# Kernel optimization log

Hardware: AMD Instinct MI355X
Metric: run time of the kernel (lower is better)

Reference implementation:

```python
import jax, jax.numpy as jnp
import numpy as np

N = 100_000      # nodes
E = 1_600_000    # edges
D = 128          # in_dim == hidden_dim
H = 4            # heads
HD = D // H      # per-head dim = 32
B = 8            # graphs in batch
TD = 128         # time_dim
NEG_SLOPE = 0.2
EPS = 1e-5


def _gelu(v):
    return jax.nn.gelu(v, approximate=False)  # torch default erf-GELU


def _layernorm(v, g, b):
    mu = jnp.mean(v, axis=-1, keepdims=True)
    var = jnp.var(v, axis=-1, keepdims=True)
    return (v - mu) * jax.lax.rsqrt(var + EPS) * g + b


def setup_inputs() -> dict:
    key = jax.random.key(0)
    ks = jax.random.split(key, 24)
    s = 1.0 / np.sqrt(D)
    inp = {
        "x": jax.random.normal(ks[0], (N, D), jnp.float32),
        "src": jax.random.randint(ks[1], (E,), 0, N),
        "dst": jax.random.randint(ks[2], (E,), 0, N),
        "graph_ids": jnp.sort(jax.random.randint(ks[3], (N,), 0, B)),
        "time_emb": jax.random.normal(ks[4], (B, TD), jnp.float32),
        # GATv2 params
        "Wsrc": jax.random.normal(ks[5], (D, D), jnp.float32) * s,
        "bsrc": jnp.zeros((D,), jnp.float32),
        "Wdst": jax.random.normal(ks[6], (D, D), jnp.float32) * s,
        "bdst": jnp.zeros((D,), jnp.float32),
        "attn": jax.random.normal(ks[7], (H, HD), jnp.float32) * (1.0 / np.sqrt(HD)),
        "gat_bias": jnp.zeros((D,), jnp.float32),
        # LayerNorms
        "ln1_g": jnp.ones((D,), jnp.float32), "ln1_b": jnp.zeros((D,), jnp.float32),
        "ln2_g": jnp.ones((D,), jnp.float32), "ln2_b": jnp.zeros((D,), jnp.float32),
        # time MLP
        "tW": jax.random.normal(ks[8], (TD, D), jnp.float32) * (1.0 / np.sqrt(TD)),
        "tb": jnp.zeros((D,), jnp.float32),
        # FFN
        "W1": jax.random.normal(ks[9], (D, 2 * D), jnp.float32) * s,
        "b1": jnp.zeros((2 * D,), jnp.float32),
        "W2": jax.random.normal(ks[10], (2 * D, D), jnp.float32) * (1.0 / np.sqrt(2 * D)),
        "b2": jnp.zeros((D,), jnp.float32),
    }
    return inp


def reference(x, src, dst, graph_ids, time_emb, Wsrc, bsrc, Wdst, bdst, attn,
              gat_bias, ln1_g, ln1_b, ln2_g, ln2_b, tW, tb, W1, b1, W2, b2):
    h = _layernorm(x, ln1_g, ln1_b)                       # [N, D]
    # GATv2Conv (share_weights=False, residual=False, activation=gelu)
    feat_src = (h @ Wsrc + bsrc).reshape(N, H, HD)        # [N, H, HD]
    feat_dst = (h @ Wdst + bdst).reshape(N, H, HD)
    e = feat_src[src] + feat_dst[dst]                     # [E, H, HD]
    e = jnp.where(e > 0, e, NEG_SLOPE * e)                # leaky_relu
    scores = jnp.einsum("ehd,hd->eh", e, attn)            # [E, H]
    # segment softmax over incoming edges of each dst node
    m = jax.ops.segment_max(scores, dst, num_segments=N)  # [N, H]
    ex = jnp.exp(scores - m[dst])
    denom = jax.ops.segment_sum(ex, dst, num_segments=N)  # [N, H]
    alpha = ex / denom[dst]                               # [E, H]
    msg = feat_src[src] * alpha[:, :, None]               # [E, H, HD]
    rst = jax.ops.segment_sum(msg, dst, num_segments=N)   # [N, H, HD]
    rst = _gelu(rst + gat_bias.reshape(H, HD))
    h = rst.reshape(N, D)                                 # flatten(1)
    # ragged time-embedding expand: time_condition[graph_of(node)]
    time_cond = _gelu(time_emb @ tW + tb)                 # [B, D]
    h = h + time_cond[graph_ids]
    h = h + x                                             # proj = Identity (in_dim == hidden_dim)
    h2 = _layernorm(h, ln2_g, ln2_b)
    h2 = _gelu(h2 @ W1 + b1) @ W2 + b2                    # FFN
    return h + h2
```

## Files before the change

### kernel.cpp

```cpp
#include <hip/hip_runtime.h>
#include <hip/hip_bf16.h>


#define RB 16
#define NEG_SLOPE 0.2f
#define LN_EPS 1e-5f

typedef __attribute__((ext_vector_type(8))) short short8v;
typedef __attribute__((ext_vector_type(4))) float floatx4;

__device__ __forceinline__ float gelu_erf(float v) {
    return 0.5f * v * (1.0f + erff(v * 0.70710678118654752f));
}
__device__ __forceinline__ unsigned short f2bf(float f) {
    unsigned int u = __float_as_uint(f);
    u += 0x7fffu + ((u >> 16) & 1u);
    return (unsigned short)(u >> 16);
}
__device__ __forceinline__ float bf2f(unsigned short u) {
    return __uint_as_float(((unsigned int)u) << 16);
}

__global__ __launch_bounds__(256) void pack_w(
    const float* __restrict__ W, unsigned short* __restrict__ P, int K, int C)
{
    int tid = blockIdx.x * 256 + threadIdx.x;
    int total = (K >> 5) * (C >> 4) * 64;
    if (tid >= total) return;
    int lane = tid & 63;
    int f = tid >> 6;
    int nkt = K >> 5;
    int nt = f / nkt, kt = f - nt * nkt;
    int col = nt * 16 + (lane & 15);
    int k0 = kt * 32 + 8 * (lane >> 4);
    short8v v;
    #pragma unroll
    for (int i = 0; i < 8; ++i)
        v[i] = (short)f2bf(W[(size_t)(k0 + i) * C + col]);
    *(short8v*)(P + (size_t)tid * 8) = v;
}

__global__ __launch_bounds__(256) void ln1_dual_gemm(
    const float* __restrict__ x,
    const float* __restrict__ ln_g, const float* __restrict__ ln_b,
    const unsigned short* __restrict__ pWs, const float* __restrict__ bsrc,
    const unsigned short* __restrict__ pWd, const float* __restrict__ bdst,
    unsigned short* __restrict__ fs, float* __restrict__ fd, int nrows)
{
    __shared__ __align__(16) float hs[RB][132];
    __shared__ __align__(16) unsigned short pa[4 * 64 * 8];
    __shared__ float s_mu[RB], s_rs[RB];

    const int tid  = threadIdx.x;
    const int row0 = blockIdx.x * RB;
    const int lane = tid & 63;
    const int w    = tid >> 6;

    #pragma unroll
    for (int i = 0; i < 2; ++i) {
        int f   = tid + i * 256;
        int row = f >> 5;
        int c0  = (f & 31) * 4;
        float4 v = make_float4(0.f, 0.f, 0.f, 0.f);
        if (row0 + row < nrows) v = *(const float4*)(x + (size_t)(row0 + row) * 128 + c0);
        *(float4*)&hs[row][c0] = v;
    }
    __syncthreads();

    {
        const int ln = lane;
        #pragma unroll
        for (int rr = 0; rr < 4; ++rr) {
            int row = w * 4 + rr;
            float v0 = hs[row][ln * 2], v1 = hs[row][ln * 2 + 1];
            float s = v0 + v1, sq = v0 * v0 + v1 * v1;
            #pragma unroll
            for (int m = 32; m; m >>= 1) { s += __shfl_xor(s, m); sq += __shfl_xor(sq, m); }
            if (ln == 0) {
                float mu  = s * (1.0f / 128.0f);
                float var = sq * (1.0f / 128.0f) - mu * mu;
                s_mu[row] = mu;
                s_rs[row] = rsqrtf(var + LN_EPS);
            }
        }
    }
    __syncthreads();

    {
        const int kt  = w;
        const int row = lane & 15;
        const int k0  = kt * 32 + 8 * (lane >> 4);
        float mu = s_mu[row], rs = s_rs[row];
        float4 u  = *(float4*)&hs[row][k0];
        float4 v  = *(float4*)&hs[row][k0 + 4];
        float4 g0 = *(const float4*)&ln_g[k0];
        float4 g1 = *(const float4*)&ln_g[k0 + 4];
        float4 c0 = *(const float4*)&ln_b[k0];
        float4 c1 = *(const float4*)&ln_b[k0 + 4];
        short8v pv;
        pv[0] = (short)f2bf((u.x - mu) * rs * g0.x + c0.x);
        pv[1] = (short)f2bf((u.y - mu) * rs * g0.y + c0.y);
        pv[2] = (short)f2bf((u.z - mu) * rs * g0.z + c0.z);
        pv[3] = (short)f2bf((u.w - mu) * rs * g0.w + c0.w);
        pv[4] = (short)f2bf((v.x - mu) * rs * g1.x + c1.x);
        pv[5] = (short)f2bf((v.y - mu) * rs * g1.y + c1.y);
        pv[6] = (short)f2bf((v.z - mu) * rs * g1.z + c1.z);
        pv[7] = (short)f2bf((v.w - mu) * rs * g1.w + c1.w);
        *(short8v*)&pa[(kt * 64 + lane) * 8] = pv;
    }
    __syncthreads();

    short8v a[4];
    #pragma unroll
    for (int kt = 0; kt < 4; ++kt)
        a[kt] = *(const short8v*)&pa[(kt * 64 + lane) * 8];

    #pragma unroll
    for (int j = 0; j < 2; ++j) {
        const int nt = 2 * w + j;
        floatx4 aS = {0.f, 0.f, 0.f, 0.f};
        floatx4 aD = {0.f, 0.f, 0.f, 0.f};
        #pragma unroll
        for (int kt = 0; kt < 4; ++kt) {
            short8v bS = *(const short8v*)(pWs + (size_t)((nt * 4 + kt) * 64 + lane) * 8);
            aS = __builtin_amdgcn_mfma_f32_16x16x32_bf16(a[kt], bS, aS, 0, 0, 0);
            short8v bD = *(const short8v*)(pWd + (size_t)((nt * 4 + kt) * 64 + lane) * 8);
            aD = __builtin_amdgcn_mfma_f32_16x16x32_bf16(a[kt], bD, aD, 0, 0, 0);
        }
        const int col = nt * 16 + (lane & 15);
        const float bS0 = bsrc[col], bD0 = bdst[col];
        #pragma unroll
        for (int r = 0; r < 4; ++r) {
            int grow = row0 + 4 * (lane >> 4) + r;
            if (grow < nrows) {
                fs[(size_t)grow * 128 + col] = f2bf(aS[r] + bS0);
                fd[(size_t)grow * 128 + col] = aD[r] + bD0;
            }
        }
    }
}

__global__ __launch_bounds__(256) void time_mlp(
    const float* __restrict__ temb, const float* __restrict__ tW,
    const float* __restrict__ tb, float* __restrict__ tc, int B)
{
    __shared__ float te[8 * 128];
    int tid = threadIdx.x;
    for (int i = tid; i < B * 128; i += 256) te[i] = temb[i];
    __syncthreads();
    int c = tid & 127, half = tid >> 7;
    for (int b = half * 4; b < half * 4 + 4; ++b) {
        if (b >= B) break;
        float acc = 0.f;
        for (int k = 0; k < 128; ++k) acc = fmaf(te[b * 128 + k], tW[k * 128 + c], acc);
        tc[b * 128 + c] = gelu_erf(acc + tb[c]);
    }
}

__global__ __launch_bounds__(256) void csr_rank(
    const int* __restrict__ dst, int* __restrict__ deg, int* __restrict__ rank, int E)
{
    int e = blockIdx.x * 256 + threadIdx.x;
    if (e < E) rank[e] = atomicAdd(&deg[dst[e]], 1);
}

__global__ __launch_bounds__(256) void scan_blocks(
    const int* __restrict__ deg, int* __restrict__ rs, int* __restrict__ btot, int N)
{
    __shared__ int wtot[4];
    const int t    = threadIdx.x;
    const int idx  = blockIdx.x * 1024 + t * 4;
    int d0 = 0, d1 = 0, d2 = 0, d3 = 0;
    if (idx + 3 < N) {
        int4 v = *(const int4*)(deg + idx);
        d0 = v.x; d1 = v.y; d2 = v.z; d3 = v.w;
    } else {
        if (idx     < N) d0 = deg[idx];
        if (idx + 1 < N) d1 = deg[idx + 1];
        if (idx + 2 < N) d2 = deg[idx + 2];
        if (idx + 3 < N) d3 = deg[idx + 3];
    }
    const int ts = d0 + d1 + d2 + d3;
    const int lane = t & 63, w = t >> 6;
    int incl = ts;
    #pragma unroll
    for (int m = 1; m < 64; m <<= 1) { int u = __shfl_up(incl, m); if (lane >= m) incl += u; }
    if (lane == 63) wtot[w] = incl;
    __syncthreads();
    int woff = 0;
    #pragma unroll
    for (int i = 0; i < 4; ++i) woff += (i < w) ? wtot[i] : 0;
    const int p = woff + incl - ts;
    if (idx + 3 < N) {
        int4 o;
        o.x = p; o.y = p + d0; o.z = p + d0 + d1; o.w = p + d0 + d1 + d2;
        *(int4*)(rs + idx) = o;
    } else {
        if (idx     < N) rs[idx]     = p;
        if (idx + 1 < N) rs[idx + 1] = p + d0;
        if (idx + 2 < N) rs[idx + 2] = p + d0 + d1;
        if (idx + 3 < N) rs[idx + 3] = p + d0 + d1 + d2;
    }
    if (t == 255) btot[blockIdx.x] = woff + incl;
}

__global__ __launch_bounds__(64) void scan_tops(
    int* __restrict__ btot, int nb, int* __restrict__ rs, int N, int E)
{
    const int lane = threadIdx.x;
    int a0 = (2 * lane     < nb) ? btot[2 * lane]     : 0;
    int a1 = (2 * lane + 1 < nb) ? btot[2 * lane + 1] : 0;
    const int ts = a0 + a1;
    int incl = ts;
    #pragma unroll
    for (int m = 1; m < 64; m <<= 1) { int u = __shfl_up(incl, m); if (lane >= m) incl += u; }
    const int ex = incl - ts;
    if (2 * lane     < nb) btot[2 * lane]     = ex;
    if (2 * lane + 1 < nb) btot[2 * lane + 1] = ex + a0;
    if (lane == 0) rs[N] = E;
}

__global__ __launch_bounds__(256) void scan_add(
    int* __restrict__ rs, const int* __restrict__ btot, int N)
{
    int i = blockIdx.x * 256 + threadIdx.x;
    if (i < N) rs[i] += btot[i >> 10];
}

__global__ __launch_bounds__(256) void csr_fill(
    const int* __restrict__ dst, const int* __restrict__ src,
    const int* __restrict__ rs, const int* __restrict__ rank,
    int* __restrict__ srcSorted, int E)
{
    int e = blockIdx.x * 256 + threadIdx.x;
    if (e < E) srcSorted[rs[dst[e]] + rank[e]] = src[e];
}

__global__ __launch_bounds__(256) void gat_gather(
    const unsigned short* __restrict__ fs, float* __restrict__ fd,
    const float* __restrict__ x,
    const int* __restrict__ srcSorted, const int* __restrict__ rs,
    const float* __restrict__ attn, const float* __restrict__ gat_bias,
    const int* __restrict__ gid, const float* __restrict__ tc, int N)
{
    const int lane = threadIdx.x & 63;
    const int wib  = threadIdx.x >> 6;
    const int n    = blockIdx.x * 4 + wib;
    if (n >= N) return;

    const int g   = lane >> 4;
    const int l16 = lane & 15;
    const int d0  = l16 * 8;

    float c1[8], c2[8], vd[8];
    {
        float4 a0 = *(const float4*)(attn + d0);
        float4 a1 = *(const float4*)(attn + d0 + 4);
        c1[0] = 0.6f * a0.x; c2[0] = 0.4f * a0.x;
        c1[1] = 0.6f * a0.y; c2[1] = 0.4f * a0.y;
        c1[2] = 0.6f * a0.z; c2[2] = 0.4f * a0.z;
        c1[3] = 0.6f * a0.w; c2[3] = 0.4f * a0.w;
        c1[4] = 0.6f * a1.x; c2[4] = 0.4f * a1.x;
        c1[5] = 0.6f * a1.y; c2[5] = 0.4f * a1.y;
        c1[6] = 0.6f * a1.z; c2[6] = 0.4f * a1.z;
        c1[7] = 0.6f * a1.w; c2[7] = 0.4f * a1.w;
        float4 v0 = *(const float4*)(fd + (size_t)n * 128 + d0);
        float4 v1 = *(const float4*)(fd + (size_t)n * 128 + d0 + 4);
        vd[0] = v0.x; vd[1] = v0.y; vd[2] = v0.z; vd[3] = v0.w;
        vd[4] = v1.x; vd[5] = v1.y; vd[6] = v1.z; vd[7] = v1.w;
    }

    const int lo = rs[n], hi = rs[n + 1];
    const int T  = (hi - lo + 3) >> 2;

    float den = 0.f;
    float w[8];
    #pragma unroll
    for (int j = 0; j < 8; ++j) w[j] = 0.f;

    int i = lo + g;
    bool vA = (i < hi);
    int sA = vA ? srcSorted[i] : 0;
    uint4 rA = *(const uint4*)(fs + (size_t)sA * 128 + d0);

    for (int t = 0; t < T; ++t) {
        const int inx = i + 4;
        const bool vB = (inx < hi);
        const int sB = vB ? srcSorted[inx] : 0;
        uint4 rB = *(const uint4*)(fs + (size_t)sB * 128 + d0);

        float v[8];
        v[0] = __uint_as_float(rA.x << 16);
        v[1] = __uint_as_float(rA.x & 0xffff0000u);
        v[2] = __uint_as_float(rA.y << 16);
        v[3] = __uint_as_float(rA.y & 0xffff0000u);
        v[4] = __uint_as_float(rA.z << 16);
        v[5] = __uint_as_float(rA.z & 0xffff0000u);
        v[6] = __uint_as_float(rA.w << 16);
        v[7] = __uint_as_float(rA.w & 0xffff0000u);

        float p = 0.f;
        #pragma unroll
        for (int j = 0; j < 8; ++j) {
            float e = v[j] + vd[j];
            p = fmaf(c1[j], e, p);
            p = fmaf(c2[j], fabsf(e), p);
        }
        p += __shfl_xor(p, 1);
        p += __shfl_xor(p, 2);
        float exv = vA ? __expf(p) : 0.f;
        den += exv;
        #pragma unroll
        for (int j = 0; j < 8; ++j) w[j] = fmaf(exv, v[j], w[j]);

        vA = vB; rA = rB; i = inx;
    }

    den += __shfl_xor(den, 16);
    den += __shfl_xor(den, 32);
    #pragma unroll
    for (int j = 0; j < 8; ++j) {
        w[j] += __shfl_xor(w[j], 16);
        w[j] += __shfl_xor(w[j], 32);
    }

    if (g == 0) {
        const float inv = den > 0.f ? 1.0f / den : 0.f;
        const int gg = gid[n];
        float4 x0 = *(const float4*)(x  + (size_t)n * 128 + d0);
        float4 x1 = *(const float4*)(x  + (size_t)n * 128 + d0 + 4);
        float4 t0 = *(const float4*)(tc + (size_t)gg * 128 + d0);
        float4 t1 = *(const float4*)(tc + (size_t)gg * 128 + d0 + 4);
        float4 g0 = *(const float4*)(gat_bias + d0);
        float4 g1 = *(const float4*)(gat_bias + d0 + 4);
        float4 o0, o1;
        o0.x = gelu_erf(w[0] * inv + g0.x) + t0.x + x0.x;
        o0.y = gelu_erf(w[1] * inv + g0.y) + t0.y + x0.y;
        o0.z = gelu_erf(w[2] * inv + g0.z) + t0.z + x0.z;
        o0.w = gelu_erf(w[3] * inv + g0.w) + t0.w + x0.w;
        o1.x = gelu_erf(w[4] * inv + g1.x) + t1.x + x1.x;
        o1.y = gelu_erf(w[5] * inv + g1.y) + t1.y + x1.y;
        o1.z = gelu_erf(w[6] * inv + g1.z) + t1.z + x1.z;
        o1.w = gelu_erf(w[7] * inv + g1.w) + t1.w + x1.w;
        *(float4*)(fd + (size_t)n * 128 + d0)     = o0;
        *(float4*)(fd + (size_t)n * 128 + d0 + 4) = o1;
    }
}

__global__ __launch_bounds__(256) void combine_ffn(
    const float* __restrict__ hmg,
    const float* __restrict__ ln_g, const float* __restrict__ ln_b,
    const unsigned short* __restrict__ pW1, const float* __restrict__ b1,
    const unsigned short* __restrict__ pW2, const float* __restrict__ b2,
    float* __restrict__ out, int nrows)
{
    __shared__ __align__(16) float hs[RB][132];
    __shared__ __align__(16) unsigned short pa[4 * 64 * 8];
    __shared__ __align__(16) unsigned short a2[RB * 264];
    __shared__ float s_mu[RB], s_rs[RB];

    const int tid  = threadIdx.x;
    const int row0 = blockIdx.x * RB;
    const int lane = tid & 63;
    const int w    = tid >> 6;

    #pragma unroll
    for (int i = 0; i < 2; ++i) {
        int f   = tid + i * 256;
        int row = f >> 5;
        int c0  = (f & 31) * 4;
        float4 v = make_float4(0.f, 0.f, 0.f, 0.f);
        if (row0 + row < nrows) v = *(const float4*)(hmg + (size_t)(row0 + row) * 128 + c0);
        *(float4*)&hs[row][c0] = v;
    }
    __syncthreads();

    {
        const int ln = lane;
        #pragma unroll
        for (int rr = 0; rr < 4; ++rr) {
            int row = w * 4 + rr;
            float v0 = hs[row][ln * 2], v1 = hs[row][ln * 2 + 1];
            float s = v0 + v1, sq = v0 * v0 + v1 * v1;
            #pragma unroll
            for (int m = 32; m; m >>= 1) { s += __shfl_xor(s, m); sq += __shfl_xor(sq, m); }
            if (ln == 0) {
                float mu  = s * (1.0f / 128.0f);
                float var = sq * (1.0f / 128.0f) - mu * mu;
                s_mu[row] = mu;
                s_rs[row] = rsqrtf(var + LN_EPS);
            }
        }
    }
    __syncthreads();

    {
        const int kt  = w;
        const int row = lane & 15;
        const int k0  = kt * 32 + 8 * (lane >> 4);
        float mu = s_mu[row], rs = s_rs[row];
        float4 u  = *(float4*)&hs[row][k0];
        float4 v  = *(float4*)&hs[row][k0 + 4];
        float4 g0 = *(const float4*)&ln_g[k0];
        float4 g1 = *(const float4*)&ln_g[k0 + 4];
        float4 c0 = *(const float4*)&ln_b[k0];
        float4 c1 = *(const float4*)&ln_b[k0 + 4];
        short8v pv;
        pv[0] = (short)f2bf((u.x - mu) * rs * g0.x + c0.x);
        pv[1] = (short)f2bf((u.y - mu) * rs * g0.y + c0.y);
        pv[2] = (short)f2bf((u.z - mu) * rs * g0.z + c0.z);
        pv[3] = (short)f2bf((u.w - mu) * rs * g0.w + c0.w);
        pv[4] = (short)f2bf((v.x - mu) * rs * g1.x + c1.x);
        pv[5] = (short)f2bf((v.y - mu) * rs * g1.y + c1.y);
        pv[6] = (short)f2bf((v.z - mu) * rs * g1.z + c1.z);
        pv[7] = (short)f2bf((v.w - mu) * rs * g1.w + c1.w);
        *(short8v*)&pa[(kt * 64 + lane) * 8] = pv;
    }
    __syncthreads();

    {
        short8v a[4];
        #pragma unroll
        for (int kt = 0; kt < 4; ++kt)
            a[kt] = *(const short8v*)&pa[(kt * 64 + lane) * 8];

        #pragma unroll
        for (int jj = 0; jj < 4; ++jj) {
            const int nt = 4 * w + jj;
            floatx4 acc = {0.f, 0.f, 0.f, 0.f};
            #pragma unroll
            for (int kt = 0; kt < 4; ++kt) {
                short8v b = *(const short8v*)(pW1 + (size_t)((nt * 4 + kt) * 64 + lane) * 8);
                acc = __builtin_amdgcn_mfma_f32_16x16x32_bf16(a[kt], b, acc, 0, 0, 0);
            }
            const int col = nt * 16 + (lane & 15);
            const float bb = b1[col];
            #pragma unroll
            for (int r = 0; r < 4; ++r) {
                int rowD = 4 * (lane >> 4) + r;
                a2[rowD * 264 + col] = f2bf(gelu_erf(acc[r] + bb));
            }
        }
    }
    __syncthreads();

    {
        floatx4 acc2[2] = {{0.f, 0.f, 0.f, 0.f}, {0.f, 0.f, 0.f, 0.f}};
        #pragma unroll
        for (int kt = 0; kt < 8; ++kt) {
            short8v af = *(const short8v*)&a2[(lane & 15) * 264 + kt * 32 + 8 * (lane >> 4)];
            #pragma unroll
            for (int j = 0; j < 2; ++j) {
                const int nt = 2 * w + j;
                short8v b = *(const short8v*)(pW2 + (size_t)((nt * 8 + kt) * 64 + lane) * 8);
                acc2[j] = __builtin_amdgcn_mfma_f32_16x16x32_bf16(af, b, acc2[j], 0, 0, 0);
            }
        }
        #pragma unroll
        for (int j = 0; j < 2; ++j) {
            const int col = (2 * w + j) * 16 + (lane & 15);
            const float bb = b2[col];
            #pragma unroll
            for (int r = 0; r < 4; ++r) {
                int rowD = 4 * (lane >> 4) + r;
                int grow = row0 + rowD;
                if (grow < nrows)
                    out[(size_t)grow * 128 + col] = hs[rowD][col] + acc2[j][r] + bb;
            }
        }
    }
}

extern "C" void kernel_launch(void* const* d_in, const int* in_sizes, int n_in,
                              void* d_out, int out_size, void* d_ws, size_t ws_size,
                              hipStream_t stream)
{
    const float* x    = (const float*)d_in[0];
    const int*   src  = (const int*)  d_in[1];
    const int*   dst  = (const int*)  d_in[2];
    const int*   gid  = (const int*)  d_in[3];
    const float* temb = (const float*)d_in[4];
    const float* Wsrc = (const float*)d_in[5];
    const float* bsrc = (const float*)d_in[6];
    const float* Wdst = (const float*)d_in[7];
    const float* bdst = (const float*)d_in[8];
    const float* attn = (const float*)d_in[9];
    const float* gbias= (const float*)d_in[10];
    const float* ln1g = (const float*)d_in[11];
    const float* ln1b = (const float*)d_in[12];
    const float* ln2g = (const float*)d_in[13];
    const float* ln2b = (const float*)d_in[14];
    const float* tW   = (const float*)d_in[15];
    const float* tb   = (const float*)d_in[16];
    const float* W1   = (const float*)d_in[17];
    const float* b1   = (const float*)d_in[18];
    const float* W2   = (const float*)d_in[19];
    const float* b2   = (const float*)d_in[20];

    const int N = in_sizes[0] / 128;
    const int E = in_sizes[1];
    const int B = in_sizes[4] / 128;
    float* out = (float*)d_out;

    char* ws = (char*)d_ws;
    size_t off = 0;
    auto alloc = [&](size_t bytes) { void* p = ws + off; off += (bytes + 255) & ~(size_t)255; return p; };
    unsigned short* fs  = (unsigned short*)alloc((size_t)N * 128 * 2);
    float* fd           = (float*)         alloc((size_t)N * 128 * 4);
    int*   deg          = (int*)           alloc((size_t)N * 4);
    int*   rsb          = (int*)           alloc((size_t)(N + 1) * 4);
    int*   rank         = (int*)           alloc((size_t)E * 4);
    int*   srcSorted    = (int*)           alloc((size_t)E * 4);
    float* tc           = (float*)         alloc((size_t)B * 128 * 4);
    int*   btot         = (int*)           alloc((size_t)1024 * 4);
    unsigned short* pWs = (unsigned short*)alloc((size_t)128 * 128 * 2);
    unsigned short* pWd = (unsigned short*)alloc((size_t)128 * 128 * 2);
    unsigned short* pW1 = (unsigned short*)alloc((size_t)128 * 256 * 2);
    unsigned short* pW2 = (unsigned short*)alloc((size_t)256 * 128 * 2);

    const int nbScan = (N + 1023) >> 10;

    hipMemsetAsync(deg, 0, (size_t)N * 4, stream);
    time_mlp<<<1, 256, 0, stream>>>(temb, tW, tb, tc, B);
    pack_w<<<(4 * 8 * 64 + 255) / 256, 256, 0, stream>>>(Wsrc, pWs, 128, 128);
    pack_w<<<(4 * 8 * 64 + 255) / 256, 256, 0, stream>>>(Wdst, pWd, 128, 128);
    pack_w<<<(4 * 16 * 64 + 255) / 256, 256, 0, stream>>>(W1, pW1, 128, 256);
    pack_w<<<(8 * 8 * 64 + 255) / 256, 256, 0, stream>>>(W2, pW2, 256, 128);
    csr_rank<<<(E + 255) / 256, 256, 0, stream>>>(dst, deg, rank, E);
    scan_blocks<<<nbScan, 256, 0, stream>>>(deg, rsb, btot, N);
    scan_tops<<<1, 64, 0, stream>>>(btot, nbScan, rsb, N, E);
    scan_add<<<(N + 255) / 256, 256, 0, stream>>>(rsb, btot, N);
    csr_fill<<<(E + 255) / 256, 256, 0, stream>>>(dst, src, rsb, rank, srcSorted, E);
    ln1_dual_gemm<<<(N + RB - 1) / RB, 256, 0, stream>>>(
        x, ln1g, ln1b, pWs, bsrc, pWd, bdst, fs, fd, N);
    gat_gather<<<(N + 3) / 4, 256, 0, stream>>>(
        fs, fd, x, srcSorted, rsb, attn, gbias, gid, tc, N);
    combine_ffn<<<(N + RB - 1) / RB, 256, 0, stream>>>(
        fd, ln2g, ln2b, pW1, b1, pW2, b2, out, N);
}
```

Before: 291.2 us.

## Merge prep kernels, store dst features in bf16, double GEMM row tiles

Folds time MLP, the four weight-pack launches and the degree memset into one prep kernel to cut launch overhead. The dst projection is now stored as bf16 instead of fp32, which halves its write and read traffic; the gather output goes to a separate fp32 buffer. The LN+GEMM and FFN kernels process 32 rows per block with two MFMA row tiles, so each loaded weight fragment is reused twice. The trade-off is lower precision on feat_dst and more registers and LDS per block.

```diff
diff --git a/kernel.cpp b/kernel.cpp
--- a/kernel.cpp
+++ b/kernel.cpp
@@ -2,7 +2,7 @@
 #include <hip/hip_bf16.h>
 
 
-#define RB 16
+#define RB2 32
 #define NEG_SLOPE 0.2f
 #define LN_EPS 1e-5f
 
@@ -17,18 +17,14 @@
     u += 0x7fffu + ((u >> 16) & 1u);
     return (unsigned short)(u >> 16);
 }
-__device__ __forceinline__ float bf2f(unsigned short u) {
-    return __uint_as_float(((unsigned int)u) << 16);
-}
-
-__global__ __launch_bounds__(256) void pack_w(
-    const float* __restrict__ W, unsigned short* __restrict__ P, int K, int C)
-{
-    int tid = blockIdx.x * 256 + threadIdx.x;
+
+__device__ __forceinline__ void pack_region(
+    const float* __restrict__ W, unsigned short* __restrict__ P, int K, int C, int idx)
+{
     int total = (K >> 5) * (C >> 4) * 64;
-    if (tid >= total) return;
-    int lane = tid & 63;
-    int f = tid >> 6;
+    if (idx >= total) return;
+    int lane = idx & 63;
+    int f = idx >> 6;
     int nkt = K >> 5;
     int nt = f / nkt, kt = f - nt * nkt;
     int col = nt * 16 + (lane & 15);
@@ -37,7 +33,50 @@
     #pragma unroll
     for (int i = 0; i < 8; ++i)
         v[i] = (short)f2bf(W[(size_t)(k0 + i) * C + col]);
-    *(short8v*)(P + (size_t)tid * 8) = v;
+    *(short8v*)(P + (size_t)idx * 8) = v;
+}
+
+__global__ __launch_bounds__(256) void prep(
+    const float* __restrict__ temb, const float* __restrict__ tW,
+    const float* __restrict__ tb, float* __restrict__ tc, int B,
+    const float* __restrict__ Wsrc, unsigned short* __restrict__ pWs,
+    const float* __restrict__ Wdst, unsigned short* __restrict__ pWd,
+    const float* __restrict__ W1,   unsigned short* __restrict__ pW1,
+    const float* __restrict__ W2,   unsigned short* __restrict__ pW2,
+    int* __restrict__ deg, int N)
+{
+    const int bid = blockIdx.x;
+    const int t   = threadIdx.x;
+    if (bid == 0) {
+        __shared__ float te[8 * 128];
+        for (int i = t; i < B * 128; i += 256) te[i] = temb[i];
+        __syncthreads();
+        int c = t & 127, half = t >> 7;
+        for (int b = half * 4; b < half * 4 + 4; ++b) {
+            if (b >= B) break;
+            float acc = 0.f;
+            for (int k = 0; k < 128; ++k) acc = fmaf(te[b * 128 + k], tW[k * 128 + c], acc);
+            tc[b * 128 + c] = gelu_erf(acc + tb[c]);
+        }
+    } else if (bid < 9) {
+        pack_region(Wsrc, pWs, 128, 128, (bid - 1) * 256 + t);
+    } else if (bid < 17) {
+        pack_region(Wdst, pWd, 128, 128, (bid - 9) * 256 + t);
+    } else if (bid < 33) {
+        pack_region(W1, pW1, 128, 256, (bid - 17) * 256 + t);
+    } else if (bid < 49) {
+        pack_region(W2, pW2, 256, 128, (bid - 33) * 256 + t);
+    } else {
+        int idx = (bid - 49) * 1024 + t * 4;
+        if (idx + 3 < N) {
+            *(int4*)(deg + idx) = make_int4(0, 0, 0, 0);
+        } else {
+            if (idx     < N) deg[idx]     = 0;
+            if (idx + 1 < N) deg[idx + 1] = 0;
+            if (idx + 2 < N) deg[idx + 2] = 0;
+            if (idx + 3 < N) deg[idx + 3] = 0;
+        }
+    }
 }
 
 __global__ __launch_bounds__(256) void ln1_dual_gemm(
@@ -45,19 +84,19 @@
     const float* __restrict__ ln_g, const float* __restrict__ ln_b,
     const unsigned short* __restrict__ pWs, const float* __restrict__ bsrc,
     const unsigned short* __restrict__ pWd, const float* __restrict__ bdst,
-    unsigned short* __restrict__ fs, float* __restrict__ fd, int nrows)
-{
-    __shared__ __align__(16) float hs[RB][132];
-    __shared__ __align__(16) unsigned short pa[4 * 64 * 8];
-    __shared__ float s_mu[RB], s_rs[RB];
+    unsigned short* __restrict__ fs, unsigned short* __restrict__ fdB, int nrows)
+{
+    __shared__ __align__(16) float hs[RB2][132];
+    __shared__ __align__(16) unsigned short pa[2][4][512];
+    __shared__ float s_mu[RB2], s_rs[RB2];
 
     const int tid  = threadIdx.x;
-    const int row0 = blockIdx.x * RB;
+    const int row0 = blockIdx.x * RB2;
     const int lane = tid & 63;
     const int w    = tid >> 6;
 
     #pragma unroll
-    for (int i = 0; i < 2; ++i) {
+    for (int i = 0; i < 4; ++i) {
         int f   = tid + i * 256;
         int row = f >> 5;
         int c0  = (f & 31) * 4;
@@ -67,29 +106,26 @@
     }
     __syncthreads();
 
-    {
-        const int ln = lane;
-        #pragma unroll
-        for (int rr = 0; rr < 4; ++rr) {
-            int row = w * 4 + rr;
-            float v0 = hs[row][ln * 2], v1 = hs[row][ln * 2 + 1];
-            float s = v0 + v1, sq = v0 * v0 + v1 * v1;
-            #pragma unroll
-            for (int m = 32; m; m >>= 1) { s += __shfl_xor(s, m); sq += __shfl_xor(sq, m); }
-            if (ln == 0) {
-                float mu  = s * (1.0f / 128.0f);
-                float var = sq * (1.0f / 128.0f) - mu * mu;
-                s_mu[row] = mu;
-                s_rs[row] = rsqrtf(var + LN_EPS);
-            }
-        }
-    }
-    __syncthreads();
-
-    {
-        const int kt  = w;
-        const int row = lane & 15;
-        const int k0  = kt * 32 + 8 * (lane >> 4);
+    #pragma unroll
+    for (int rr = 0; rr < 8; ++rr) {
+        int row = w * 8 + rr;
+        float v0 = hs[row][lane * 2], v1 = hs[row][lane * 2 + 1];
+        float s = v0 + v1, sq = v0 * v0 + v1 * v1;
+        #pragma unroll
+        for (int m = 32; m; m >>= 1) { s += __shfl_xor(s, m); sq += __shfl_xor(sq, m); }
+        if (lane == 0) {
+            float mu  = s * (1.0f / 128.0f);
+            float var = sq * (1.0f / 128.0f) - mu * mu;
+            s_mu[row] = mu;
+            s_rs[row] = rsqrtf(var + LN_EPS);
+        }
+    }
+    __syncthreads();
+
+    #pragma unroll
+    for (int rt = 0; rt < 2; ++rt) {
+        const int row = rt * 16 + (lane & 15);
+        const int k0  = w * 32 + 8 * (lane >> 4);
         float mu = s_mu[row], rs = s_rs[row];
         float4 u  = *(float4*)&hs[row][k0];
         float4 v  = *(float4*)&hs[row][k0 + 4];
@@ -106,54 +142,45 @@
         pv[5] = (short)f2bf((v.y - mu) * rs * g1.y + c1.y);
         pv[6] = (short)f2bf((v.z - mu) * rs * g1.z + c1.z);
         pv[7] = (short)f2bf((v.w - mu) * rs * g1.w + c1.w);
-        *(short8v*)&pa[(kt * 64 + lane) * 8] = pv;
-    }
-    __syncthreads();
-
-    short8v a[4];
-    #pragma unroll
-    for (int kt = 0; kt < 4; ++kt)
-        a[kt] = *(const short8v*)&pa[(kt * 64 + lane) * 8];
+        *(short8v*)&pa[rt][w][lane * 8] = pv;
+    }
+    __syncthreads();
+
+    short8v a[2][4];
+    #pragma unroll
+    for (int rt = 0; rt < 2; ++rt)
+        #pragma unroll
+        for (int kt = 0; kt < 4; ++kt)
+            a[rt][kt] = *(const short8v*)&pa[rt][kt][lane * 8];
 
     #pragma unroll
     for (int j = 0; j < 2; ++j) {
         const int nt = 2 * w + j;
-        floatx4 aS = {0.f, 0.f, 0.f, 0.f};
-        floatx4 aD = {0.f, 0.f, 0.f, 0.f};
+        floatx4 aS[2] = {{0.f,0.f,0.f,0.f},{0.f,0.f,0.f,0.f}};
+        floatx4 aD[2] = {{0.f,0.f,0.f,0.f},{0.f,0.f,0.f,0.f}};
         #pragma unroll
         for (int kt = 0; kt < 4; ++kt) {
             short8v bS = *(const short8v*)(pWs + (size_t)((nt * 4 + kt) * 64 + lane) * 8);
-            aS = __builtin_amdgcn_mfma_f32_16x16x32_bf16(a[kt], bS, aS, 0, 0, 0);
             short8v bD = *(const short8v*)(pWd + (size_t)((nt * 4 + kt) * 64 + lane) * 8);
-            aD = __builtin_amdgcn_mfma_f32_16x16x32_bf16(a[kt], bD, aD, 0, 0, 0);
+            #pragma unroll
+            for (int rt = 0; rt < 2; ++rt) {
+                aS[rt] = __builtin_amdgcn_mfma_f32_16x16x32_bf16(a[rt][kt], bS, aS[rt], 0, 0, 0);
+                aD[rt] = __builtin_amdgcn_mfma_f32_16x16x32_bf16(a[rt][kt], bD, aD[rt], 0, 0, 0);
+            }
         }
         const int col = nt * 16 + (lane & 15);
         const float bS0 = bsrc[col], bD0 = bdst[col];
         #pragma unroll
-        for (int r = 0; r < 4; ++r) {
-            int grow = row0 + 4 * (lane >> 4) + r;
-            if (grow < nrows) {
-                fs[(size_t)grow * 128 + col] = f2bf(aS[r] + bS0);
-                fd[(size_t)grow * 128 + col] = aD[r] + bD0;
+        for (int rt = 0; rt < 2; ++rt) {
+            #pragma unroll
+            for (int r = 0; r < 4; ++r) {
+                int grow = row0 + rt * 16 + 4 * (lane >> 4) + r;
+                if (grow < nrows) {
+                    fs [(size_t)grow * 128 + col] = f2bf(aS[rt][r] + bS0);
+                    fdB[(size_t)grow * 128 + col] = f2bf(aD[rt][r] + bD0);
+                }
             }
         }
-    }
-}
-
-__global__ __launch_bounds__(256) void time_mlp(
-    const float* __restrict__ temb, const float* __restrict__ tW,
-    const float* __restrict__ tb, float* __restrict__ tc, int B)
-{
-    __shared__ float te[8 * 128];
-    int tid = threadIdx.x;
-    for (int i = tid; i < B * 128; i += 256) te[i] = temb[i];
-    __syncthreads();
-    int c = tid & 127, half = tid >> 7;
-    for (int b = half * 4; b < half * 4 + 4; ++b) {
-        if (b >= B) break;
-        float acc = 0.f;
-        for (int k = 0; k < 128; ++k) acc = fmaf(te[b * 128 + k], tW[k * 128 + c], acc);
-        tc[b * 128 + c] = gelu_erf(acc + tb[c]);
     }
 }
 
@@ -237,8 +264,8 @@
 }
 
 __global__ __launch_bounds__(256) void gat_gather(
-    const unsigned short* __restrict__ fs, float* __restrict__ fd,
-    const float* __restrict__ x,
+    const unsigned short* __restrict__ fs, const unsigned short* __restrict__ fdB,
+    float* __restrict__ hm, const float* __restrict__ x,
     const int* __restrict__ srcSorted, const int* __restrict__ rs,
     const float* __restrict__ attn, const float* __restrict__ gat_bias,
     const int* __restrict__ gid, const float* __restrict__ tc, int N)
@@ -264,10 +291,15 @@
         c1[5] = 0.6f * a1.y; c2[5] = 0.4f * a1.y;
         c1[6] = 0.6f * a1.z; c2[6] = 0.4f * a1.z;
         c1[7] = 0.6f * a1.w; c2[7] = 0.4f * a1.w;
-        float4 v0 = *(const float4*)(fd + (size_t)n * 128 + d0);
-        float4 v1 = *(const float4*)(fd + (size_t)n * 128 + d0 + 4);
-        vd[0] = v0.x; vd[1] = v0.y; vd[2] = v0.z; vd[3] = v0.w;
-        vd[4] = v1.x; vd[5] = v1.y; vd[6] = v1.z; vd[7] = v1.w;
+        uint4 vdu = *(const uint4*)(fdB + (size_t)n * 128 + d0);
+        vd[0] = __uint_as_float(vdu.x << 16);
+        vd[1] = __uint_as_float(vdu.x & 0xffff0000u);
+        vd[2] = __uint_as_float(vdu.y << 16);
+        vd[3] = __uint_as_float(vdu.y & 0xffff0000u);
+        vd[4] = __uint_as_float(vdu.z << 16);
+        vd[5] = __uint_as_float(vdu.z & 0xffff0000u);
+        vd[6] = __uint_as_float(vdu.w << 16);
+        vd[7] = __uint_as_float(vdu.w & 0xffff0000u);
     }
 
     const int lo = rs[n], hi = rs[n + 1];
@@ -342,8 +374,8 @@
         o1.y = gelu_erf(w[5] * inv + g1.y) + t1.y + x1.y;
         o1.z = gelu_erf(w[6] * inv + g1.z) + t1.z + x1.z;
         o1.w = gelu_erf(w[7] * inv + g1.w) + t1.w + x1.w;
-        *(float4*)(fd + (size_t)n * 128 + d0)     = o0;
-        *(float4*)(fd + (size_t)n * 128 + d0 + 4) = o1;
+        *(float4*)(hm + (size_t)n * 128 + d0)     = o0;
+        *(float4*)(hm + (size_t)n * 128 + d0 + 4) = o1;
     }
 }
 
@@ -354,18 +386,18 @@
     const unsigned short* __restrict__ pW2, const float* __restrict__ b2,
     float* __restrict__ out, int nrows)
 {
-    __shared__ __align__(16) float hs[RB][132];
-    __shared__ __align__(16) unsigned short pa[4 * 64 * 8];
-    __shared__ __align__(16) unsigned short a2[RB * 264];
-    __shared__ float s_mu[RB], s_rs[RB];
+    __shared__ __align__(16) float hs[RB2][132];
+    __shared__ __align__(16) unsigned short pa[2][4][512];
+    __shared__ __align__(16) unsigned short a2[RB2][264];
+    __shared__ float s_mu[RB2], s_rs[RB2];
 
     const int tid  = threadIdx.x;
-    const int row0 = blockIdx.x * RB;
+    const int row0 = blockIdx.x * RB2;
     const int lane = tid & 63;
     const int w    = tid >> 6;
 
     #pragma unroll
-    for (int i = 0; i < 2; ++i) {
+    for (int i = 0; i < 4; ++i) {
         int f   = tid + i * 256;
         int row = f >> 5;
         int c0  = (f & 31) * 4;
@@ -375,29 +407,26 @@
     }
     __syncthreads();
 
-    {
-        const int ln = lane;
-        #pragma unroll
-        for (int rr = 0; rr < 4; ++rr) {
-            int row = w * 4 + rr;
-            float v0 = hs[row][ln * 2], v1 = hs[row][ln * 2 + 1];
-            float s = v0 + v1, sq = v0 * v0 + v1 * v1;
-            #pragma unroll
-            for (int m = 32; m; m >>= 1) { s += __shfl_xor(s, m); sq += __shfl_xor(sq, m); }
-            if (ln == 0) {
-                float mu  = s * (1.0f / 128.0f);
-                float var = sq * (1.0f / 128.0f) - mu * mu;
-                s_mu[row] = mu;
-                s_rs[row] = rsqrtf(var + LN_EPS);
-            }
-        }
-    }
-    __syncthreads();
-
-    {
-        const int kt  = w;
-        const int row = lane & 15;
-        const int k0  = kt * 32 + 8 * (lane >> 4);
+    #pragma unroll
+    for (int rr = 0; rr < 8; ++rr) {
+        int row = w * 8 + rr;
+        float v0 = hs[row][lane * 2], v1 = hs[row][lane * 2 + 1];
+        float s = v0 + v1, sq = v0 * v0 + v1 * v1;
+        #pragma unroll
+        for (int m = 32; m; m >>= 1) { s += __shfl_xor(s, m); sq += __shfl_xor(sq, m); }
+        if (lane == 0) {
+            float mu  = s * (1.0f / 128.0f);
+            float var = sq * (1.0f / 128.0f) - mu * mu;
+            s_mu[row] = mu;
+            s_rs[row] = rsqrtf(var + LN_EPS);
+        }
+    }
+    __syncthreads();
+
+    #pragma unroll
+    for (int rt = 0; rt < 2; ++rt) {
+        const int row = rt * 16 + (lane & 15);
+        const int k0  = w * 32 + 8 * (lane >> 4);
         float mu = s_mu[row], rs = s_rs[row];
         float4 u  = *(float4*)&hs[row][k0];
         float4 v  = *(float4*)&hs[row][k0 + 4];
@@ -414,46 +443,56 @@
         pv[5] = (short)f2bf((v.y - mu) * rs * g1.y + c1.y);
         pv[6] = (short)f2bf((v.z - mu) * rs * g1.z + c1.z);
         pv[7] = (short)f2bf((v.w - mu) * rs * g1.w + c1.w);
-        *(short8v*)&pa[(kt * 64 + lane) * 8] = pv;
+        *(short8v*)&pa[rt][w][lane * 8] = pv;
     }
     __syncthreads();
 
     {
-        short8v a[4];
-        #pragma unroll
-        for (int kt = 0; kt < 4; ++kt)
-            a[kt] = *(const short8v*)&pa[(kt * 64 + lane) * 8];
+        short8v a[2][4];
+        #pragma unroll
+        for (int rt = 0; rt < 2; ++rt)
+            #pragma unroll
+            for (int kt = 0; kt < 4; ++kt)
+                a[rt][kt] = *(const short8v*)&pa[rt][kt][lane * 8];
 
         #pragma unroll
         for (int jj = 0; jj < 4; ++jj) {
             const int nt = 4 * w + jj;
-            floatx4 acc = {0.f, 0.f, 0.f, 0.f};
+            floatx4 acc[2] = {{0.f,0.f,0.f,0.f},{0.f,0.f,0.f,0.f}};
             #pragma unroll
             for (int kt = 0; kt < 4; ++kt) {
                 short8v b = *(const short8v*)(pW1 + (size_t)((nt * 4 + kt) * 64 + lane) * 8);
-                acc = __builtin_amdgcn_mfma_f32_16x16x32_bf16(a[kt], b, acc, 0, 0, 0);
+                #pragma unroll
+                for (int rt = 0; rt < 2; ++rt)
+                    acc[rt] = __builtin_amdgcn_mfma_f32_16x16x32_bf16(a[rt][kt], b, acc[rt], 0, 0, 0);
             }
             const int col = nt * 16 + (lane & 15);
             const float bb = b1[col];
             #pragma unroll
-            for (int r = 0; r < 4; ++r) {
-                int rowD = 4 * (lane >> 4) + r;
-                a2[rowD * 264 + col] = f2bf(gelu_erf(acc[r] + bb));
-            }
+            for (int rt = 0; rt < 2; ++rt)
+                #pragma unroll
+                for (int r = 0; r < 4; ++r)
+                    a2[rt * 16 + 4 * (lane >> 4) + r][col] = f2bf(gelu_erf(acc[rt][r] + bb));
         }
     }
     __syncthreads();
 
     {
-        floatx4 acc2[2] = {{0.f, 0.f, 0.f, 0.f}, {0.f, 0.f, 0.f, 0.f}};
+        floatx4 acc2[2][2] = {{{0.f,0.f,0.f,0.f},{0.f,0.f,0.f,0.f}},
+                              {{0.f,0.f,0.f,0.f},{0.f,0.f,0.f,0.f}}};
         #pragma unroll
         for (int kt = 0; kt < 8; ++kt) {
-            short8v af = *(const short8v*)&a2[(lane & 15) * 264 + kt * 32 + 8 * (lane >> 4)];
+            short8v af[2];
+            #pragma unroll
+            for (int rt = 0; rt < 2; ++rt)
+                af[rt] = *(const short8v*)&a2[rt * 16 + (lane & 15)][kt * 32 + 8 * (lane >> 4)];
             #pragma unroll
             for (int j = 0; j < 2; ++j) {
                 const int nt = 2 * w + j;
                 short8v b = *(const short8v*)(pW2 + (size_t)((nt * 8 + kt) * 64 + lane) * 8);
-                acc2[j] = __builtin_amdgcn_mfma_f32_16x16x32_bf16(af, b, acc2[j], 0, 0, 0);
+                #pragma unroll
+                for (int rt = 0; rt < 2; ++rt)
+                    acc2[j][rt] = __builtin_amdgcn_mfma_f32_16x16x32_bf16(af[rt], b, acc2[j][rt], 0, 0, 0);
             }
         }
         #pragma unroll
@@ -461,12 +500,14 @@
             const int col = (2 * w + j) * 16 + (lane & 15);
             const float bb = b2[col];
             #pragma unroll
-            for (int r = 0; r < 4; ++r) {
-                int rowD = 4 * (lane >> 4) + r;
-                int grow = row0 + rowD;
-                if (grow < nrows)
-                    out[(size_t)grow * 128 + col] = hs[rowD][col] + acc2[j][r] + bb;
-            }
+            for (int rt = 0; rt < 2; ++rt)
+                #pragma unroll
+                for (int r = 0; r < 4; ++r) {
+                    int rowD = rt * 16 + 4 * (lane >> 4) + r;
+                    int grow = row0 + rowD;
+                    if (grow < nrows)
+                        out[(size_t)grow * 128 + col] = hs[rowD][col] + acc2[j][rt][r] + bb;
+                }
         }
     }
 }
@@ -506,7 +547,8 @@
     size_t off = 0;
     auto alloc = [&](size_t bytes) { void* p = ws + off; off += (bytes + 255) & ~(size_t)255; return p; };
     unsigned short* fs  = (unsigned short*)alloc((size_t)N * 128 * 2);
-    float* fd           = (float*)         alloc((size_t)N * 128 * 4);
+    unsigned short* fdB = (unsigned short*)alloc((size_t)N * 128 * 2);
+    float* hm           = (float*)         alloc((size_t)N * 128 * 4);
     int*   deg          = (int*)           alloc((size_t)N * 4);
     int*   rsb          = (int*)           alloc((size_t)(N + 1) * 4);
     int*   rank         = (int*)           alloc((size_t)E * 4);
@@ -519,22 +561,19 @@
     unsigned short* pW2 = (unsigned short*)alloc((size_t)256 * 128 * 2);
 
     const int nbScan = (N + 1023) >> 10;
-
-    hipMemsetAsync(deg, 0, (size_t)N * 4, stream);
-    time_mlp<<<1, 256, 0, stream>>>(temb, tW, tb, tc, B);
-    pack_w<<<(4 * 8 * 64 + 255) / 256, 256, 0, stream>>>(Wsrc, pWs, 128, 128);
-    pack_w<<<(4 * 8 * 64 + 255) / 256, 256, 0, stream>>>(Wdst, pWd, 128, 128);
-    pack_w<<<(4 * 16 * 64 + 255) / 256, 256, 0, stream>>>(W1, pW1, 128, 256);
-    pack_w<<<(8 * 8 * 64 + 255) / 256, 256, 0, stream>>>(W2, pW2, 256, 128);
+    const int nbZero = (N + 1023) >> 10;
+
+    prep<<<49 + nbZero, 256, 0, stream>>>(temb, tW, tb, tc, B,
+        Wsrc, pWs, Wdst, pWd, W1, pW1, W2, pW2, deg, N);
     csr_rank<<<(E + 255) / 256, 256, 0, stream>>>(dst, deg, rank, E);
     scan_blocks<<<nbScan, 256, 0, stream>>>(deg, rsb, btot, N);
     scan_tops<<<1, 64, 0, stream>>>(btot, nbScan, rsb, N, E);
     scan_add<<<(N + 255) / 256, 256, 0, stream>>>(rsb, btot, N);
     csr_fill<<<(E + 255) / 256, 256, 0, stream>>>(dst, src, rsb, rank, srcSorted, E);
-    ln1_dual_gemm<<<(N + RB - 1) / RB, 256, 0, stream>>>(
-        x, ln1g, ln1b, pWs, bsrc, pWd, bdst, fs, fd, N);
+    ln1_dual_gemm<<<(N + RB2 - 1) / RB2, 256, 0, stream>>>(
+        x, ln1g, ln1b, pWs, bsrc, pWd, bdst, fs, fdB, N);
     gat_gather<<<(N + 3) / 4, 256, 0, stream>>>(
-        fs, fd, x, srcSorted, rsb, attn, gbias, gid, tc, N);
-    combine_ffn<<<(N + RB - 1) / RB, 256, 0, stream>>>(
-        fd, ln2g, ln2b, pW1, b1, pW2, b2, out, N);
-}
+        fs, fdB, hm, x, srcSorted, rsb, attn, gbias, gid, tc, N);
+    combine_ffn<<<(N + RB2 - 1) / RB2, 256, 0, stream>>>(
+        hm, ln2g, ln2b, pW1, b1, pW2, b2, out, N);
+}
```

Measured after the change: 293.4 us. No clear change (+0.8%).
